# Kernel tuning notes

Measured on AMD Instinct MI355X. Metric: run time of the kernel, lower is better.

The kernel has to match this reference:

```python
import jax, jax.numpy as jnp
import numpy as np

D_MODEL = 512
N_STATE = 512  # must equal D_MODEL (torch code broadcasts B*(N,) against u[:,t] of (batch,d_model))
BATCH = 8
SEQ_LEN = 4096
DT_MIN, DT_MAX = 0.001, 0.1


def setup_inputs() -> dict:
    key = jax.random.key(0)
    k_u, k_lam, k_b, k_q, k_dt = jax.random.split(key, 5)
    u = jax.random.normal(k_u, (BATCH, SEQ_LEN, D_MODEL), dtype=jnp.float32)
    Lambda = jax.random.normal(k_lam, (N_STATE,), dtype=jnp.float32)
    B = jax.random.normal(k_b, (N_STATE,), dtype=jnp.float32)
    Q = jax.random.normal(k_q, (N_STATE, D_MODEL), dtype=jnp.float32) / np.sqrt(N_STATE)
    log_dt = jax.random.uniform(k_dt, (1,), dtype=jnp.float32) * (np.log(DT_MAX) - np.log(DT_MIN)) + np.log(DT_MIN)
    return {"u": u, "Lambda": Lambda, "B": B, "Q": Q, "log_dt": log_dt}


def reference(u, Lambda, B, Q, log_dt):
    # dt = exp(log_dt); A = diag(exp(dt * -exp(Lambda))) -> x @ A.T == x * a
    dt = jnp.exp(log_dt)              # (1,)
    a = jnp.exp(dt * (-jnp.exp(Lambda)))  # (N,)
    Bdt = dt * B                      # (N,)

    u_t = jnp.transpose(u, (1, 0, 2))  # (L, batch, N)

    def step(x, ut):
        x = x * a + Bdt * ut           # diagonal recurrence, (batch, N)
        return x, x

    x0 = jnp.zeros((u.shape[0], Lambda.shape[0]), dtype=u.dtype)
    _, xs = jax.lax.scan(step, x0, u_t)       # (L, batch, N)
    y = jnp.einsum('lbn,nd->bld', xs, Q)      # project to d_model
    return y
```

## Files before the change

kernel.cpp:

```cpp
#include <hip/hip_runtime.h>
#include <hip/hip_bf16.h>

#define BATCH 8
#define SEQ   4096
#define NST   512
#define DM    512
#define NCHUNK 64
#define TCH    64
#define LDP    (NST + 8)

typedef __attribute__((ext_vector_type(4))) float f32x4;
typedef __attribute__((ext_vector_type(2))) float f32x2;
typedef __attribute__((ext_vector_type(8))) short short8v;
typedef __attribute__((ext_vector_type(4))) short short4v;

__device__ __forceinline__ short f2bf(float f) {
  union { float f; unsigned u; } v; v.f = f;
  unsigned r = v.u + 0x7FFFu + ((v.u >> 16) & 1u);
  return (short)(r >> 16);
}

__global__ void k_scan_sums(const float* __restrict__ u, const float* __restrict__ Lam,
                            const float* __restrict__ Bv, const float* __restrict__ log_dt,
                            float* __restrict__ S) {
  int gid = blockIdx.x * 256 + threadIdx.x;
  int n2 = (gid & 255) * 2;
  int bc = gid >> 8;
  int b  = bc & (BATCH - 1);
  int c  = bc >> 3;
  float dt = expf(log_dt[0]);
  f32x2 lam = *(const f32x2*)(Lam + n2);
  f32x2 bv  = *(const f32x2*)(Bv + n2);
  float a0 = expf(-dt * expf(lam[0])), a1 = expf(-dt * expf(lam[1]));
  float g0 = dt * bv[0],               g1 = dt * bv[1];
  const float* up = u + ((size_t)b * SEQ + (size_t)c * TCH) * NST + n2;
  float s0 = 0.f, s1 = 0.f;
  #pragma unroll 8
  for (int t = 0; t < TCH; ++t) {
    f32x2 v = *(const f32x2*)(up + (size_t)t * NST);
    s0 = fmaf(a0, s0, g0 * v[0]);
    s1 = fmaf(a1, s1, g1 * v[1]);
  }
  *(f32x2*)(S + (c * BATCH + b) * NST + n2) = (f32x2){s0, s1};
}

__global__ void k_propagate(const float* __restrict__ Lam, const float* __restrict__ log_dt,
                            const float* __restrict__ S, float* __restrict__ Xc) {
  int gid = blockIdx.x * 256 + threadIdx.x;
  int n = gid & (NST - 1);
  int b = gid >> 9;
  float dt = expf(log_dt[0]);
  float a  = expf(-dt * expf(Lam[n]));
  float aT = a;
  #pragma unroll
  for (int i = 0; i < 6; ++i) aT *= aT;
  float x = 0.f;
  for (int c = 0; c < NCHUNK; ++c) {
    Xc[(c * BATCH + b) * NST + n] = x;
    x = fmaf(aT, x, S[(c * BATCH + b) * NST + n]);
  }
}

__global__ void k_transQ(const float* __restrict__ Q, short* __restrict__ Qt) {
  __shared__ short tile[64][68];
  int bn = (blockIdx.x & 7) * 64;
  int bd = (blockIdx.x >> 3) * 64;
  int tc = threadIdx.x & 15;
  int tr = threadIdx.x >> 4;
  #pragma unroll
  for (int i = 0; i < 4; ++i) {
    int r = tr + i * 16;
    f32x4 v = *(const f32x4*)(Q + (size_t)(bn + r) * DM + bd + tc * 4);
    short4v h;
    h[0] = f2bf(v[0]); h[1] = f2bf(v[1]); h[2] = f2bf(v[2]); h[3] = f2bf(v[3]);
    *(short4v*)&tile[r][tc * 4] = h;
  }
  __syncthreads();
  #pragma unroll
  for (int i = 0; i < 4; ++i) {
    int r = tr + i * 16;
    short4v h;
    #pragma unroll
    for (int j = 0; j < 4; ++j) h[j] = tile[tc * 4 + j][r];
    *(short4v*)(Qt + (size_t)(bd + r) * NST + bn + tc * 4) = h;
  }
}

__global__ __launch_bounds__(512) void k_fused(
    const float* __restrict__ u, const float* __restrict__ Lam,
    const float* __restrict__ Bv, const float* __restrict__ log_dt,
    const float* __restrict__ Xc, const short* __restrict__ Qt,
    float* __restrict__ y) {
  __shared__ __align__(16) short X[TCH][LDP];
  const int tid = threadIdx.x;
  const int b = blockIdx.x & (BATCH - 1);
  const int c = blockIdx.x >> 3;

  {
    const float dt = expf(log_dt[0]);
    const float a  = expf(-dt * expf(Lam[tid]));
    const float g  = dt * Bv[tid];
    float x  = Xc[(c * BATCH + b) * NST + tid];
    const float* up = u + ((size_t)b * SEQ + (size_t)c * TCH) * NST + tid;
    float ur[TCH];
    #pragma unroll
    for (int t = 0; t < TCH; ++t) ur[t] = up[(size_t)t * NST];
    #pragma unroll
    for (int t = 0; t < TCH; ++t) {
      x = fmaf(a, x, g * ur[t]);
      X[t][tid] = f2bf(x);
    }
  }
  __syncthreads();

  const int lane = tid & 63;
  const int wc   = tid >> 6;
  const int l15  = lane & 15;
  const int lhi  = lane >> 4;
  const int ka   = lhi * 8;
  const short* qbase = Qt + (size_t)(wc * 64 + l15) * NST + ka;
  float* yb = y + ((size_t)b * SEQ + (size_t)c * TCH) * DM;

  f32x4 acc[4][4];
  #pragma unroll
  for (int mi = 0; mi < 4; ++mi)
    #pragma unroll
    for (int nf = 0; nf < 4; ++nf) acc[mi][nf] = (f32x4){0.f, 0.f, 0.f, 0.f};

  #pragma unroll 4
  for (int kk = 0; kk < 16; ++kk) {
    const int k0 = kk * 32;
    short8v afrag[4];
    #pragma unroll
    for (int mi = 0; mi < 4; ++mi)
      afrag[mi] = *(const short8v*)&X[mi * 16 + l15][k0 + ka];
    short8v bfrag[4];
    #pragma unroll
    for (int nf = 0; nf < 4; ++nf)
      bfrag[nf] = *(const short8v*)(qbase + (size_t)nf * 16 * NST + k0);
    #pragma unroll
    for (int mi = 0; mi < 4; ++mi)
      #pragma unroll
      for (int nf = 0; nf < 4; ++nf)
        acc[mi][nf] = __builtin_amdgcn_mfma_f32_16x16x32_bf16(afrag[mi], bfrag[nf], acc[mi][nf], 0, 0, 0);
  }

  #pragma unroll
  for (int mi = 0; mi < 4; ++mi)
    #pragma unroll
    for (int nf = 0; nf < 4; ++nf) {
      const int rr = mi * 16 + lhi * 4;
      const int cc = wc * 64 + nf * 16 + l15;
      #pragma unroll
      for (int i = 0; i < 4; ++i)
        yb[(size_t)(rr + i) * DM + cc] = acc[mi][nf][i];
    }
}

extern "C" void kernel_launch(void* const* d_in, const int* in_sizes, int n_in,
                              void* d_out, int out_size, void* d_ws, size_t ws_size,
                              hipStream_t stream) {
  const float* u      = (const float*)d_in[0];
  const float* Lam    = (const float*)d_in[1];
  const float* Bv     = (const float*)d_in[2];
  const float* Q      = (const float*)d_in[3];
  const float* log_dt = (const float*)d_in[4];
  float* out = (float*)d_out;

  float* S  = (float*)d_ws;
  float* Xc = S + NCHUNK * BATCH * NST;
  short* Qt = (short*)(Xc + NCHUNK * BATCH * NST);

  hipLaunchKernelGGL(k_transQ, dim3(64), dim3(256), 0, stream, Q, Qt);
  hipLaunchKernelGGL(k_scan_sums, dim3(NCHUNK * BATCH), dim3(256), 0, stream,
                     u, Lam, Bv, log_dt, S);
  hipLaunchKernelGGL(k_propagate, dim3(BATCH * NST / 256), dim3(256), 0, stream,
                     Lam, log_dt, S, Xc);
  hipLaunchKernelGGL(k_fused, dim3(NCHUNK * BATCH), dim3(512), 0, stream,
                     u, Lam, Bv, log_dt, Xc, Qt, out);
}
```

Before: 69.97 us.

## Split per-chunk scan into four sub-chunks with vectorized float4 loads

Result: no change. 70.79 us (+1.2%).

```diff
diff --git a/kernel.cpp b/kernel.cpp
--- a/kernel.cpp
+++ b/kernel.cpp
@@ -7,10 +7,11 @@
 #define DM    512
 #define NCHUNK 64
 #define TCH    64
+#define NSUB   4
+#define RSUB   16
 #define LDP    (NST + 8)
 
 typedef __attribute__((ext_vector_type(4))) float f32x4;
-typedef __attribute__((ext_vector_type(2))) float f32x2;
 typedef __attribute__((ext_vector_type(8))) short short8v;
 typedef __attribute__((ext_vector_type(4))) short short4v;
 
@@ -23,25 +24,26 @@
 __global__ void k_scan_sums(const float* __restrict__ u, const float* __restrict__ Lam,
                             const float* __restrict__ Bv, const float* __restrict__ log_dt,
                             float* __restrict__ S) {
-  int gid = blockIdx.x * 256 + threadIdx.x;
-  int n2 = (gid & 255) * 2;
-  int bc = gid >> 8;
+  int gid = blockIdx.x * 128 + threadIdx.x;
+  int n0 = (gid & 127) * 4;
+  int bc = gid >> 7;
   int b  = bc & (BATCH - 1);
   int c  = bc >> 3;
   float dt = expf(log_dt[0]);
-  f32x2 lam = *(const f32x2*)(Lam + n2);
-  f32x2 bv  = *(const f32x2*)(Bv + n2);
-  float a0 = expf(-dt * expf(lam[0])), a1 = expf(-dt * expf(lam[1]));
-  float g0 = dt * bv[0],               g1 = dt * bv[1];
-  const float* up = u + ((size_t)b * SEQ + (size_t)c * TCH) * NST + n2;
-  float s0 = 0.f, s1 = 0.f;
+  f32x4 lam = *(const f32x4*)(Lam + n0);
+  f32x4 bv  = *(const f32x4*)(Bv + n0);
+  float a[4], g[4];
+  #pragma unroll
+  for (int i = 0; i < 4; ++i) { a[i] = expf(-dt * expf(lam[i])); g[i] = dt * bv[i]; }
+  const float* up = u + ((size_t)b * SEQ + (size_t)c * TCH) * NST + n0;
+  f32x4 s = (f32x4){0.f, 0.f, 0.f, 0.f};
   #pragma unroll 8
   for (int t = 0; t < TCH; ++t) {
-    f32x2 v = *(const f32x2*)(up + (size_t)t * NST);
-    s0 = fmaf(a0, s0, g0 * v[0]);
-    s1 = fmaf(a1, s1, g1 * v[1]);
-  }
-  *(f32x2*)(S + (c * BATCH + b) * NST + n2) = (f32x2){s0, s1};
+    f32x4 v = *(const f32x4*)(up + (size_t)t * NST);
+    #pragma unroll
+    for (int i = 0; i < 4; ++i) s[i] = fmaf(a[i], s[i], g[i] * v[i]);
+  }
+  *(f32x4*)(S + (c * BATCH + b) * NST + n0) = s;
 }
 
 __global__ void k_propagate(const float* __restrict__ Lam, const float* __restrict__ log_dt,
@@ -92,23 +94,69 @@
     const float* __restrict__ Xc, const short* __restrict__ Qt,
     float* __restrict__ y) {
   __shared__ __align__(16) short X[TCH][LDP];
+  __shared__ __align__(16) float Ssub[NSUB][NST];
   const int tid = threadIdx.x;
   const int b = blockIdx.x & (BATCH - 1);
   const int c = blockIdx.x >> 3;
+  const int tq = tid >> 7;
+  const int q  = tid & 127;
+  const int n0 = q * 4;
 
   {
     const float dt = expf(log_dt[0]);
-    const float a  = expf(-dt * expf(Lam[tid]));
-    const float g  = dt * Bv[tid];
-    float x  = Xc[(c * BATCH + b) * NST + tid];
-    const float* up = u + ((size_t)b * SEQ + (size_t)c * TCH) * NST + tid;
-    float ur[TCH];
-    #pragma unroll
-    for (int t = 0; t < TCH; ++t) ur[t] = up[(size_t)t * NST];
-    #pragma unroll
-    for (int t = 0; t < TCH; ++t) {
-      x = fmaf(a, x, g * ur[t]);
-      X[t][tid] = f2bf(x);
+    f32x4 lam = *(const f32x4*)(Lam + n0);
+    f32x4 bv  = *(const f32x4*)(Bv + n0);
+    float a[4], g[4], a16[4];
+    #pragma unroll
+    for (int i = 0; i < 4; ++i) {
+      a[i] = expf(-dt * expf(lam[i]));
+      g[i] = dt * bv[i];
+      float t = a[i]; t *= t; t *= t; t *= t; t *= t;
+      a16[i] = t;
+    }
+    f32x4 seed = (f32x4){0.f, 0.f, 0.f, 0.f};
+    if (tq == 0) seed = *(const f32x4*)(Xc + (c * BATCH + b) * NST + n0);
+
+    const float* up = u + ((size_t)b * SEQ + (size_t)(c * TCH + tq * RSUB)) * NST + n0;
+    f32x4 v[RSUB];
+    #pragma unroll
+    for (int j = 0; j < RSUB; ++j) v[j] = *(const f32x4*)(up + (size_t)j * NST);
+
+    f32x4 x = seed;
+    #pragma unroll
+    for (int j = 0; j < RSUB; ++j) {
+      #pragma unroll
+      for (int i = 0; i < 4; ++i) x[i] = fmaf(a[i], x[i], g[i] * v[j][i]);
+      v[j] = x;
+    }
+    *(f32x4*)&Ssub[tq][n0] = x;
+    __syncthreads();
+
+    if (tq > 0) {
+      f32x4 I = *(const f32x4*)&Ssub[0][n0];
+      for (int s = 1; s < tq; ++s) {
+        f32x4 sv = *(const f32x4*)&Ssub[s][n0];
+        #pragma unroll
+        for (int i = 0; i < 4; ++i) I[i] = fmaf(a16[i], I[i], sv[i]);
+      }
+      f32x4 ap;
+      #pragma unroll
+      for (int i = 0; i < 4; ++i) ap[i] = a[i];
+      #pragma unroll
+      for (int j = 0; j < RSUB; ++j) {
+        #pragma unroll
+        for (int i = 0; i < 4; ++i) {
+          v[j][i] = fmaf(ap[i], I[i], v[j][i]);
+          ap[i] *= a[i];
+        }
+      }
+    }
+    #pragma unroll
+    for (int j = 0; j < RSUB; ++j) {
+      short4v h;
+      h[0] = f2bf(v[j][0]); h[1] = f2bf(v[j][1]);
+      h[2] = f2bf(v[j][2]); h[3] = f2bf(v[j][3]);
+      *(short4v*)&X[tq * RSUB + j][n0] = h;
     }
   }
   __syncthreads();
@@ -172,7 +220,7 @@
   short* Qt = (short*)(Xc + NCHUNK * BATCH * NST);
 
   hipLaunchKernelGGL(k_transQ, dim3(64), dim3(256), 0, stream, Q, Qt);
-  hipLaunchKernelGGL(k_scan_sums, dim3(NCHUNK * BATCH), dim3(256), 0, stream,
+  hipLaunchKernelGGL(k_scan_sums, dim3(NCHUNK * BATCH), dim3(128), 0, stream,
                      u, Lam, Bv, log_dt, S);
   hipLaunchKernelGGL(k_propagate, dim3(BATCH * NST / 256), dim3(256), 0, stream,
                      Lam, log_dt, S, Xc);
```
